# Optimization experiments

Measured on AMD Instinct MI355X. Metric: run time of the kernel, lower is better.

Reference implementation:

```python
import jax, jax.numpy as jnp
import numpy as np
from jax import lax

SR = 7
HEADS = 8
EPS = 1e-5

def dwconv(x, w):
    # x: [B,C,H,W], w: [C,1,3,3] depthwise
    return lax.conv_general_dilated(x, w, (1, 1), 'SAME',
                                    feature_group_count=x.shape[1],
                                    dimension_numbers=('NCHW', 'OIHW', 'NCHW'))

def bn(x, g, b, m, v):
    # eval-mode BatchNorm2d over channel dim of [B,C,H,W]
    scale = g / jnp.sqrt(v + EPS)
    return x * scale[:, None, None] + (b - m * scale)[:, None, None]

def avgpool(x, k):
    B, C, H, W = x.shape
    return x.reshape(B, C, H // k, k, W // k, k).mean(axis=(3, 5))

def upsample(x, k):
    B, C, H, W = x.shape
    return jax.image.resize(x, (B, C, H * k, W * k), method='bilinear')


def setup_inputs() -> dict:
    key = jax.random.key(0)
    ks = jax.random.split(key, 12)
    B, N, C = 16, 3136, 256
    d = {}
    d['x'] = jax.random.normal(ks[0], (B, N, C), jnp.float32)
    d['Wv'] = jax.random.normal(ks[1], (C, C), jnp.float32) * 0.05
    d['conv1_w'] = jax.random.normal(ks[2], (C, 1, 3, 3), jnp.float32) * 0.05
    d['bn1_g'] = jnp.ones((C,), jnp.float32)
    d['bn1_b'] = jnp.zeros((C,), jnp.float32)
    d['bn1_m'] = jax.random.normal(ks[3], (C,), jnp.float32) * 0.05
    d['bn1_v'] = jax.random.uniform(ks[4], (C,), jnp.float32, 0.5, 1.5)
    d['conv2_w'] = jax.random.normal(ks[5], (C, 1, 3, 3), jnp.float32) * 0.05
    d['bn2_g'] = jnp.ones((C,), jnp.float32)
    d['bn2_b'] = jnp.zeros((C,), jnp.float32)
    d['bn2_m'] = jax.random.normal(ks[6], (C,), jnp.float32) * 0.05
    d['bn2_v'] = jax.random.uniform(ks[7], (C,), jnp.float32, 0.5, 1.5)
    d['vup_w'] = jax.random.normal(ks[8], (C, 1, 3, 3), jnp.float32) * 0.05
    d['bn3_g'] = jnp.ones((C,), jnp.float32)
    d['bn3_b'] = jnp.zeros((C,), jnp.float32)
    d['bn3_m'] = jax.random.normal(ks[9], (C,), jnp.float32) * 0.05
    d['bn3_v'] = jax.random.uniform(ks[10], (C,), jnp.float32, 0.5, 1.5)
    d['Wp'] = jax.random.normal(ks[11], (C, C), jnp.float32) * 0.05
    d['bp'] = jnp.zeros((C,), jnp.float32)
    return d


def reference(x, Wv, conv1_w, bn1_g, bn1_b, bn1_m, bn1_v,
              conv2_w, bn2_g, bn2_b, bn2_m, bn2_v,
              vup_w, bn3_g, bn3_b, bn3_m, bn3_v, Wp, bp):
    B, N, C = x.shape
    h = w = int(np.sqrt(N))
    hd = C // HEADS
    scale = C ** (-0.5)

    v = x @ Wv.T                                    # [B,N,C] (torch Linear, no bias)
    skip = v.reshape(B, h, w, C).transpose(0, 3, 1, 2)  # [B,C,h,w]

    s1 = bn(dwconv(skip, conv1_w), bn1_g, bn1_b, bn1_m, bn1_v)
    q = avgpool(s1, SR)                             # [B,C,h_,w_]
    s2 = bn(dwconv(jax.nn.gelu(s1, approximate=False), conv2_w),
            bn2_g, bn2_b, bn2_m, bn2_v)
    k = avgpool(s2, SR)                             # [B,C,h_,w_]
    skip_tok = jax.nn.gelu(s2, approximate=False).reshape(B, C, N).transpose(0, 2, 1)

    h_, w_ = h // SR, w // SR
    N_ = h_ * w_
    qh = q.reshape(B, HEADS, hd, N_).transpose(0, 1, 3, 2)   # [B,H,N_,d]
    kh = k.reshape(B, HEADS, hd, N_).transpose(0, 1, 3, 2)   # [B,H,N_,d]
    vh = v.reshape(B, N, HEADS, hd).transpose(0, 2, 1, 3)    # [B,H,N,d]

    attn = jnp.einsum('bhnd,bhmd->bhnm', qh, kh)             # [B,H,N_,N_]
    attn = attn.reshape(B * HEADS, N_, h_, w_)
    attn = upsample(attn, SR) * scale                        # [B*H,N_,h,w]
    attn = attn.reshape(B, HEADS, N_, N)
    attn = jax.nn.softmax(attn, axis=-1)

    o = jnp.einsum('bhnm,bhmd->bhnd', attn, vh)              # [B,H,N_,d]
    o = o.reshape(B, HEADS, h_, w_, hd).transpose(0, 1, 4, 2, 3).reshape(B, C, h_, w_)
    o = bn(dwconv(upsample(o, SR), vup_w), bn3_g, bn3_b, bn3_m, bn3_v)  # [B,C,h,w]

    out = o.reshape(B, C, N).transpose(0, 2, 1) + skip_tok
    out = out @ Wp.T + bp
    return out
```

## Files before the change

### kernel.cpp

```cpp
#include <hip/hip_runtime.h>
#include <math.h>

#define B_     16
#define H_IMG  56
#define W_IMG  56
#define N_TOK  3136
#define C_     256
#define C4_    64
#define NHEAD  8
#define HDIM   32
#define NCH    8

typedef float f32x4 __attribute__((ext_vector_type(4)));
typedef __bf16 bf16x8 __attribute__((ext_vector_type(8)));

__device__ __forceinline__ float geluf(float x) {
    return 0.5f * x * (1.0f + erff(x * 0.70710678118654752f));
}

__device__ __forceinline__ void up_coef(int o, int& i0, int& i1, float& t) {
    float f  = (float)(o - 3) * (1.0f / 7.0f);
    float fl = floorf(f);
    int   ii = (int)fl;
    t = f - fl;
    if (ii < 0)       { i0 = 0; i1 = 0; t = 0.0f; }
    else if (ii >= 7) { i0 = 7; i1 = 7; t = 0.0f; }
    else              { i0 = ii; i1 = ii + 1; }
}

__device__ __forceinline__ void split_bf16(float4 f, uint2& hi, uint2& lo) {
    unsigned u0 = __float_as_uint(f.x), u1 = __float_as_uint(f.y);
    unsigned u2 = __float_as_uint(f.z), u3 = __float_as_uint(f.w);
    unsigned h0 = u0 & 0xFFFF0000u, h1 = u1 & 0xFFFF0000u;
    unsigned h2 = u2 & 0xFFFF0000u, h3 = u3 & 0xFFFF0000u;
    hi = make_uint2((h0 >> 16) | h1, (h2 >> 16) | h3);
    float l0 = f.x - __uint_as_float(h0);
    float l1 = f.y - __uint_as_float(h1);
    float l2 = f.z - __uint_as_float(h2);
    float l3 = f.w - __uint_as_float(h3);
    lo = make_uint2((__float_as_uint(l0) >> 16) | (__float_as_uint(l1) & 0xFFFF0000u),
                    (__float_as_uint(l2) >> 16) | (__float_as_uint(l3) & 0xFFFF0000u));
}

__device__ __forceinline__ unsigned pack2_bf16(float a, float b) {
    __bf16 ha = (__bf16)a, hb = (__bf16)b;
    unsigned short ua = __builtin_bit_cast(unsigned short, ha);
    unsigned short ub = __builtin_bit_cast(unsigned short, hb);
    return (unsigned)ua | ((unsigned)ub << 16);
}

__device__ __forceinline__ void gload_lds16(const float* g, float* l) {
    __builtin_amdgcn_global_load_lds(
        (const __attribute__((address_space(1))) unsigned int*)g,
        (__attribute__((address_space(3))) unsigned int*)l, 16, 0, 0);
}

__global__ void prep_kernel(
    const float* __restrict__ w1, const float* __restrict__ w2, const float* __restrict__ w3,
    const float* __restrict__ g1, const float* __restrict__ b1, const float* __restrict__ m1, const float* __restrict__ v1,
    const float* __restrict__ g2, const float* __restrict__ b2, const float* __restrict__ m2, const float* __restrict__ v2,
    const float* __restrict__ g3, const float* __restrict__ b3, const float* __restrict__ m3, const float* __restrict__ v3,
    float* __restrict__ wT1, float* __restrict__ wT2, float* __restrict__ wT3,
    float* __restrict__ sc1, float* __restrict__ sh1,
    float* __restrict__ sc2, float* __restrict__ sh2,
    float* __restrict__ sc3, float* __restrict__ sh3)
{
    int c = threadIdx.x;
#pragma unroll
    for (int t = 0; t < 9; ++t) {
        wT1[t * C_ + c] = w1[c * 9 + t];
        wT2[t * C_ + c] = w2[c * 9 + t];
        wT3[t * C_ + c] = w3[c * 9 + t];
    }
    float s1 = g1[c] * rsqrtf(v1[c] + 1e-5f); sc1[c] = s1; sh1[c] = b1[c] - m1[c] * s1;
    float s2 = g2[c] * rsqrtf(v2[c] + 1e-5f); sc2[c] = s2; sh2[c] = b2[c] - m2[c] * s2;
    float s3 = g3[c] * rsqrtf(v3[c] + 1e-5f); sc3[c] = s3; sh3[c] = b3[c] - m3[c] * s3;
}

__global__ __launch_bounds__(256, 2) void gemm_nt_mfma_kernel(
    const float* __restrict__ A,
    const float* __restrict__ Bm,
    const float* __restrict__ bias,
    float* __restrict__ C,
    int M, int N)
{
    __shared__ float lds[8192];
    const int tid  = threadIdx.x;
    const int nb   = N >> 7;
    const int nwg  = (M >> 7) * nb;
    const int cpx  = nwg >> 3;
    const int bid  = blockIdx.x;
    const int swz  = (bid & 7) * cpx + (bid >> 3);
    const int bx   = swz % nb;
    const int by   = swz / nb;
    const int lane = tid & 63;
    const int wv   = tid >> 6;
    const int wr   = wv >> 1, wc = wv & 1;
    const int l15  = lane & 15, kb = lane >> 4;

    const float* Abase = A  + (size_t)(by * 128) * 256;
    const float* Bbase = Bm + (size_t)(bx * 128) * 256;

    f32x4 acc[4][4];
#pragma unroll
    for (int m = 0; m < 4; ++m)
#pragma unroll
        for (int n = 0; n < 4; ++n) acc[m][n] = (f32x4)(0.0f);

    int srow[4], ssk[4];
#pragma unroll
    for (int i = 0; i < 4; ++i) {
        int u = i * 256 + tid;
        srow[i] = u >> 3;
        ssk[i]  = ((u & 7) ^ (srow[i] & 7)) << 2;
    }

#pragma unroll
    for (int k0 = 0; k0 < 256; k0 += 32) {
        __syncthreads();
#pragma unroll
        for (int i = 0; i < 4; ++i) {
            int u = i * 256 + tid;
            gload_lds16(Abase + (size_t)srow[i] * 256 + k0 + ssk[i], &lds[u * 4]);
        }
#pragma unroll
        for (int i = 0; i < 4; ++i) {
            int u = i * 256 + tid;
            gload_lds16(Bbase + (size_t)srow[i] * 256 + k0 + ssk[i], &lds[4096 + u * 4]);
        }
        __syncthreads();

        bf16x8 ah[4], al[4], bh[4], bl[4];
#pragma unroll
        for (int m = 0; m < 4; ++m) {
            int r = wr * 64 + m * 16 + l15;
            float4 f0 = *(const float4*)&lds[r * 32 + ((((kb * 2)    ) ^ (r & 7)) << 2)];
            float4 f1 = *(const float4*)&lds[r * 32 + ((((kb * 2) + 1) ^ (r & 7)) << 2)];
            uint2 h0, l0, h1, l1;
            split_bf16(f0, h0, l0);
            split_bf16(f1, h1, l1);
            ah[m] = __builtin_bit_cast(bf16x8, make_uint4(h0.x, h0.y, h1.x, h1.y));
            al[m] = __builtin_bit_cast(bf16x8, make_uint4(l0.x, l0.y, l1.x, l1.y));
        }
#pragma unroll
        for (int n = 0; n < 4; ++n) {
            int r = wc * 64 + n * 16 + l15;
            float4 f0 = *(const float4*)&lds[4096 + r * 32 + ((((kb * 2)    ) ^ (r & 7)) << 2)];
            float4 f1 = *(const float4*)&lds[4096 + r * 32 + ((((kb * 2) + 1) ^ (r & 7)) << 2)];
            uint2 h0, l0, h1, l1;
            split_bf16(f0, h0, l0);
            split_bf16(f1, h1, l1);
            bh[n] = __builtin_bit_cast(bf16x8, make_uint4(h0.x, h0.y, h1.x, h1.y));
            bl[n] = __builtin_bit_cast(bf16x8, make_uint4(l0.x, l0.y, l1.x, l1.y));
        }
#pragma unroll
        for (int m = 0; m < 4; ++m)
#pragma unroll
            for (int n = 0; n < 4; ++n) {
                acc[m][n] = __builtin_amdgcn_mfma_f32_16x16x32_bf16(ah[m], bh[n], acc[m][n], 0, 0, 0);
                acc[m][n] = __builtin_amdgcn_mfma_f32_16x16x32_bf16(ah[m], bl[n], acc[m][n], 0, 0, 0);
                acc[m][n] = __builtin_amdgcn_mfma_f32_16x16x32_bf16(al[m], bh[n], acc[m][n], 0, 0, 0);
            }
    }

    const int rb = by * 128 + wr * 64 + kb * 4;
    const int cb = bx * 128 + wc * 64 + l15;
#pragma unroll
    for (int n = 0; n < 4; ++n) {
        int col = cb + n * 16;
        float bv = bias ? bias[col] : 0.0f;
#pragma unroll
        for (int m = 0; m < 4; ++m) {
            int row = rb + m * 16;
#pragma unroll
            for (int r = 0; r < 4; ++r)
                C[(size_t)(row + r) * N + col] = acc[m][n][r] + bv;
        }
    }
}

__global__ __launch_bounds__(256, 4) void dwconv_bn_pool_gelu_kernel(
    const float* __restrict__ in, const float* __restrict__ wT,
    const float* __restrict__ scv, const float* __restrict__ shv,
    float* __restrict__ outg, float* __restrict__ pool)
{
    const int blk = blockIdx.x;
    const int xcd = blk & 7;
    const int j   = blk >> 3;
    const int b   = xcd + 8 * (j >> 6);
    const int g   = j & 63;
    const int gy  = g >> 3, gx = g & 7;
    const int tid = threadIdx.x;
    const int c4  = tid & 63;
    const int wv  = tid >> 6;
    const int c0  = c4 * 4;

    float4 wr[9];
#pragma unroll
    for (int t = 0; t < 9; ++t) wr[t] = *(const float4*)(wT + t * C_ + c0);
    const float4 sc = *(const float4*)(scv + c0);
    const float4 sh = *(const float4*)(shv + c0);

    const int x0 = gx * 7, y0 = gy * 7;
    const float* inb = in + (size_t)b * N_TOK * C_;
    float4 acc = make_float4(0, 0, 0, 0);

    for (int p = wv; p < 49; p += 4) {
        int py = p / 7, px = p - py * 7;
        int y = y0 + py, x = x0 + px;
        float cx = 0.f, cy = 0.f, cz = 0.f, cw = 0.f;
#pragma unroll
        for (int dy = -1; dy <= 1; ++dy) {
            int yy = y + dy;
            if (yy < 0 || yy >= H_IMG) continue;
#pragma unroll
            for (int dx = -1; dx <= 1; ++dx) {
                int xx = x + dx;
                if (xx < 0 || xx >= W_IMG) continue;
                const float4 iv = *(const float4*)(inb + (size_t)(yy * W_IMG + xx) * C_ + c0);
                const float4 w  = wr[(dy + 1) * 3 + (dx + 1)];
                cx = fmaf(iv.x, w.x, cx);
                cy = fmaf(iv.y, w.y, cy);
                cz = fmaf(iv.z, w.z, cz);
                cw = fmaf(iv.w, w.w, cw);
            }
        }
        float vx = cx * sc.x + sh.x;
        float vy = cy * sc.y + sh.y;
        float vz = cz * sc.z + sh.z;
        float vw = cw * sc.w + sh.w;
        acc.x += vx; acc.y += vy; acc.z += vz; acc.w += vw;
        *(float4*)(outg + ((size_t)b * N_TOK + y * W_IMG + x) * C_ + c0) =
            make_float4(geluf(vx), geluf(vy), geluf(vz), geluf(vw));
    }

    __shared__ float4 ps[4][64];
    ps[wv][c4] = acc;
    __syncthreads();
    if (tid < 64) {
        float4 s  = ps[0][tid];
        float4 t1 = ps[1][tid];
        float4 t2 = ps[2][tid];
        float4 t3 = ps[3][tid];
        const float r = 1.0f / 49.0f;
        *(float4*)(pool + ((size_t)b * 64 + g) * C_ + tid * 4) = make_float4(
            (s.x + t1.x + t2.x + t3.x) * r, (s.y + t1.y + t2.y + t3.y) * r,
            (s.z + t1.z + t2.z + t3.z) * r, (s.w + t1.w + t2.w + t3.w) * r);
    }
}

__global__ __launch_bounds__(256, 3) void dwconv_up_bn_add_kernel(
    const float* __restrict__ osm,
    const float* __restrict__ wT,
    const float* __restrict__ scv, const float* __restrict__ shv,
    const float* __restrict__ add_,
    float* __restrict__ out)
{
    const int blk = blockIdx.x;
    const int xcd = blk & 7;
    const int j   = blk >> 3;
    const int b   = xcd + 8 * (j >> 6);
    const int g   = j & 63;
    const int gy  = g >> 3, gx = g & 7;
    const int tid = threadIdx.x;
    const int c4  = tid & 63;
    const int wv  = tid >> 6;
    const int c0  = c4 * 4;

    float4 wr[9];
#pragma unroll
    for (int t = 0; t < 9; ++t) wr[t] = *(const float4*)(wT + t * C_ + c0);
    const float4 sc = *(const float4*)(scv + c0);
    const float4 sh = *(const float4*)(shv + c0);

    const float* ob = osm + (size_t)b * 64 * C_ + c0;
    const int cry0 = max(gy - 1, 0), cry2 = min(gy + 1, 7);
    const int crx0 = max(gx - 1, 0), crx2 = min(gx + 1, 7);
    float4 P[3][3];
#pragma unroll
    for (int ri = 0; ri < 3; ++ri) {
        const int rowc = (ri == 0) ? cry0 : ((ri == 1) ? gy : cry2);
        P[ri][0] = *(const float4*)(ob + (size_t)(rowc * 8 + crx0) * C_);
        P[ri][1] = *(const float4*)(ob + (size_t)(rowc * 8 + gx)   * C_);
        P[ri][2] = *(const float4*)(ob + (size_t)(rowc * 8 + crx2) * C_);
    }

    for (int cpass = 0; cpass < 2; ++cpass) {
        const int xi = wv + cpass * 4;
        if (xi >= 7) break;
        const int x = gx * 7 + xi;

        float axw[3][3];
#pragma unroll
        for (int e = 0; e < 3; ++e) {
            int xx = x - 1 + e;
            if (xx >= 0 && xx < W_IMG) {
                int i0, i1; float t;
                up_coef(xx, i0, i1, t);
                const bool r0 = (i0 - gx + 1) == 0;
                axw[e][0] = r0 ? (1.0f - t) : 0.0f;
                axw[e][1] = r0 ? t : (1.0f - t);
                axw[e][2] = r0 ? 0.0f : t;
            } else {
                axw[e][0] = 0.0f; axw[e][1] = 0.0f; axw[e][2] = 0.0f;
            }
        }

        float4 S[3][3];
#pragma unroll
        for (int d = 0; d < 3; ++d) {
            float4 cw0, cw1, cw2;
#pragma unroll
            for (int ci = 0; ci < 3; ++ci) {
                float4 c;
                c.x = wr[d*3+0].x * axw[0][ci] + wr[d*3+1].x * axw[1][ci] + wr[d*3+2].x * axw[2][ci];
                c.y = wr[d*3+0].y * axw[0][ci] + wr[d*3+1].y * axw[1][ci] + wr[d*3+2].y * axw[2][ci];
                c.z = wr[d*3+0].z * axw[0][ci] + wr[d*3+1].z * axw[1][ci] + wr[d*3+2].z * axw[2][ci];
                c.w = wr[d*3+0].w * axw[0][ci] + wr[d*3+1].w * axw[1][ci] + wr[d*3+2].w * axw[2][ci];
                if (ci == 0) cw0 = c; else if (ci == 1) cw1 = c; else cw2 = c;
            }
#pragma unroll
            for (int ri = 0; ri < 3; ++ri) {
                float4 s;
                s.x = cw0.x * P[ri][0].x + cw1.x * P[ri][1].x + cw2.x * P[ri][2].x;
                s.y = cw0.y * P[ri][0].y + cw1.y * P[ri][1].y + cw2.y * P[ri][2].y;
                s.z = cw0.z * P[ri][0].z + cw1.z * P[ri][1].z + cw2.z * P[ri][2].z;
                s.w = cw0.w * P[ri][0].w + cw1.w * P[ri][1].w + cw2.w * P[ri][2].w;
                S[d][ri] = s;
            }
        }

#pragma unroll
        for (int y7 = 0; y7 < 7; ++y7) {
            const int y = gy * 7 + y7;
            float ax = 0.f, ay = 0.f, az = 0.f, aw = 0.f;
#pragma unroll
            for (int d = 0; d < 3; ++d) {
                const int yy = y + d - 1;
                if (yy < 0 || yy >= H_IMG) continue;
                int i0, i1; float ty;
                up_coef(yy, i0, i1, ty);
                const bool hi2 = (i0 - gy + 1) != 0;
                const float4 lo = hi2 ? S[d][1] : S[d][0];
                const float4 hi = hi2 ? S[d][2] : S[d][1];
                ax += fmaf(ty, hi.x - lo.x, lo.x);
                ay += fmaf(ty, hi.y - lo.y, lo.y);
                az += fmaf(ty, hi.z - lo.z, lo.z);
                aw += fmaf(ty, hi.w - lo.w, lo.w);
            }
            const size_t pix = (size_t)b * N_TOK + (size_t)y * W_IMG + x;
            const float4 av = *(const float4*)(add_ + pix * C_ + c0);
            *(float4*)(out + pix * C_ + c0) = make_float4(
                ax * sc.x + sh.x + av.x, ay * sc.y + sh.y + av.y,
                az * sc.z + sh.z + av.z, aw * sc.w + sh.w + av.w);
        }
    }
}

__global__ __launch_bounds__(256) void qk_kernel(
    const float* __restrict__ q, const float* __restrict__ k,
    float* __restrict__ attnL, float* __restrict__ mrow_g)
{
    int bh = blockIdx.x;
    int b = bh >> 3, head = bh & 7;
    __shared__ float qs[64][33];
    __shared__ float ks[64][33];
    int tid = threadIdx.x;
    for (int t = tid; t < 512; t += 256) {
        int i = t >> 3, dq = (t & 7) * 4;
        const float4 qv = *(const float4*)(q + ((size_t)(b * 64 + i) * C_ + head * 32 + dq));
        const float4 kv = *(const float4*)(k + ((size_t)(b * 64 + i) * C_ + head * 32 + dq));
        qs[i][dq + 0] = qv.x; qs[i][dq + 1] = qv.y; qs[i][dq + 2] = qv.z; qs[i][dq + 3] = qv.w;
        ks[i][dq + 0] = kv.x; ks[i][dq + 1] = kv.y; ks[i][dq + 2] = kv.z; ks[i][dq + 3] = kv.w;
    }
    __syncthreads();
    int i  = tid >> 2;
    int jb = (tid & 3) * 16;
    float qr[32];
#pragma unroll
    for (int d = 0; d < 32; ++d) qr[d] = qs[i][d];
    float* outp = attnL + (size_t)bh * 4096 + i * 64 + jb;
    float mloc = -1e30f;
#pragma unroll
    for (int j = 0; j < 16; ++j) {
        float s = 0.f;
#pragma unroll
        for (int d = 0; d < 32; ++d) s = fmaf(qr[d], ks[jb + j][d], s);
        float sv = s * 0.0625f;
        outp[j] = sv;
        mloc = fmaxf(mloc, sv);
    }
    mloc = fmaxf(mloc, __shfl_xor(mloc, 1));
    mloc = fmaxf(mloc, __shfl_xor(mloc, 2));
    if ((tid & 3) == 0) mrow_g[bh * 64 + i] = mloc;
}

#define S_ALS 0
#define S_P   1792
#define S_VH  4096
#define S_VL  5248
#define S_RY  6400
#define S_ZP  7168
__global__ __launch_bounds__(256, 4) void attn_pv_kernel(
    const float* __restrict__ attnL,
    const float* __restrict__ mrow_g,
    const float* __restrict__ v,
    float* __restrict__ part_o,
    float* __restrict__ part_z)
{
    __shared__ unsigned sm[7424];
    float* smf = (float*)sm;

    const int blk   = blockIdx.x;
    const int xcd   = blk & 7;
    const int r8    = blk >> 3;
    const int b     = xcd + 8 * (r8 >> 6);
    const int rem   = r8 & 63;
    const int head  = rem >> 3;
    const int chunk = rem & 7;
    const int bh    = b * 8 + head;
    const int jb    = min(max(chunk - 1, 0), 5);

    const int tid  = threadIdx.x;
    const int lane = tid & 63;
    const int w    = tid >> 6;
    const int l15  = lane & 15, kb = lane >> 4;
    const int i    = tid >> 2;
    const int dg   = tid & 3;

    for (int u = tid; u < 384; u += 256) {
        int row = u / 6, cc = u % 6;
        float4 va = *(const float4*)(attnL + (size_t)bh * 4096 + row * 64 + jb * 8 + cc * 4);
        *(float4*)&smf[S_ALS + row * 28 + cc * 4] = va;
    }
    sm[S_P + (tid >> 2) * 36 + 28 + (tid & 3)] = 0;
    {
        int base = (tid < 128) ? S_VH : S_VL;
        int q2 = tid & 127;
        sm[base + (q2 >> 2) * 36 + 28 + (q2 & 3)] = 0;
    }
    const float mr = mrow_g[bh * 64 + i];

    int   x0a[14]; float txa[14];
#pragma unroll
    for (int j = 0; j < 14; ++j) {
        int i0, i1; float t;
        up_coef(dg * 14 + j, i0, i1, t);
        x0a[j] = i0; txa[j] = t;
    }

    f32x4 acc[2];
    acc[0] = (f32x4)(0.0f); acc[1] = (f32x4)(0.0f);
    float zacc = 0.0f;

    for (int rr = 0; rr < 7; ++rr) {
        const int y = chunk * 7 + rr;
        __syncthreads();

        float4 va, vb;
        if (tid < 224) {
            int x2 = tid >> 3, d0 = (tid & 7) * 4;
            const float* vp = v + ((size_t)b * N_TOK + y * W_IMG + 2 * x2) * C_ + head * 32 + d0;
            va = *(const float4*)vp;
            vb = *(const float4*)(vp + C_);
        }
        {
            int y0, y1; float ty;
            up_coef(y, y0, y1, ty);
#pragma unroll
            for (int kk2 = dg; kk2 < 9; kk2 += 4) {
                int ks2 = kk2 < 8 ? kk2 : 7;
                float a0 = smf[S_ALS + i * 28 + (y0 - jb) * 8 + ks2];
                float a1 = smf[S_ALS + i * 28 + (y1 - jb) * 8 + ks2];
                smf[S_RY + i * 12 + kk2] = fmaf(ty, a1 - a0, a0) - mr;
            }
        }
        if (tid < 224) {
            int x2 = tid >> 3, d0 = (tid & 7) * 4;
            float ae[4] = {va.x, va.y, va.z, va.w};
            float be[4] = {vb.x, vb.y, vb.z, vb.w};
#pragma unroll
            for (int j = 0; j < 4; ++j) {
                unsigned ua = __float_as_uint(ae[j]), ha = ua & 0xFFFF0000u;
                unsigned ub = __float_as_uint(be[j]), hb2 = ub & 0xFFFF0000u;
                sm[S_VH + (d0 + j) * 36 + x2] = (ha >> 16) | hb2;
                float la = ae[j] - __uint_as_float(ha);
                float lb = be[j] - __uint_as_float(hb2);
                sm[S_VL + (d0 + j) * 36 + x2] =
                    (__float_as_uint(la) >> 16) | (__float_as_uint(lb) & 0xFFFF0000u);
            }
        }
        __syncthreads();

#pragma unroll
        for (int j = 0; j < 7; ++j) {
            float r0 = smf[S_RY + i * 12 + x0a[2 * j]];
            float r1 = smf[S_RY + i * 12 + x0a[2 * j] + 1];
            float l0 = fmaf(txa[2 * j], r1 - r0, r0);
            float r2 = smf[S_RY + i * 12 + x0a[2 * j + 1]];
            float r3 = smf[S_RY + i * 12 + x0a[2 * j + 1] + 1];
            float l1 = fmaf(txa[2 * j + 1], r3 - r2, r2);
            float p0 = __expf(l0), p1 = __expf(l1);
            zacc += p0 + p1;
            sm[S_P + i * 36 + dg * 7 + j] = pack2_bf16(p0, p1);
        }
        __syncthreads();

#pragma unroll
        for (int s = 0; s < 2; ++s) {
            bf16x8 pa = *(const bf16x8*)&sm[S_P + (w * 16 + l15) * 36 + s * 16 + kb * 4];
#pragma unroll
            for (int n = 0; n < 2; ++n) {
                bf16x8 bhv = *(const bf16x8*)&sm[S_VH + (n * 16 + l15) * 36 + s * 16 + kb * 4];
                bf16x8 blv = *(const bf16x8*)&sm[S_VL + (n * 16 + l15) * 36 + s * 16 + kb * 4];
                acc[n] = __builtin_amdgcn_mfma_f32_16x16x32_bf16(pa, bhv, acc[n], 0, 0, 0);
                acc[n] = __builtin_amdgcn_mfma_f32_16x16x32_bf16(pa, blv, acc[n], 0, 0, 0);
            }
        }
    }

    smf[S_ZP + i * 4 + dg] = zacc;
    __syncthreads();
    if (tid < 64) {
        float zt = smf[S_ZP + tid * 4] + smf[S_ZP + tid * 4 + 1] +
                   smf[S_ZP + tid * 4 + 2] + smf[S_ZP + tid * 4 + 3];
        part_z[((size_t)bh * NCH + chunk) * 64 + tid] = zt;
    }
    const int row4 = (lane >> 4) * 4;
#pragma unroll
    for (int n = 0; n < 2; ++n)
#pragma unroll
        for (int r2 = 0; r2 < 4; ++r2) {
            int i2 = w * 16 + row4 + r2;
            int d  = n * 16 + l15;
            part_o[(((size_t)bh * NCH + chunk) * 64 + i2) * 32 + d] = acc[n][r2];
        }
}

__global__ __launch_bounds__(256) void combine_kernel(
    const float* __restrict__ part_o, const float* __restrict__ part_z,
    float* __restrict__ o_small)
{
    int idx = blockIdx.x * 256 + threadIdx.x;
    if (idx >= B_ * 64 * C_) return;
    int c = idx % C_;
    int g = (idx / C_) % 64;
    int b = idx / (C_ * 64);
    int head = c >> 5, d = c & 31;
    int bh = b * 8 + head;
    float oo = 0.f, zz = 0.f;
    for (int ch = 0; ch < NCH; ++ch) {
        oo += part_o[(((size_t)bh * NCH + ch) * 64 + g) * 32 + d];
        zz += part_z[((size_t)bh * NCH + ch) * 64 + g];
    }
    o_small[idx] = oo / zz;
}

extern "C" void kernel_launch(void* const* d_in, const int* in_sizes, int n_in,
                              void* d_out, int out_size, void* d_ws, size_t ws_size,
                              hipStream_t stream)
{
    const float* x    = (const float*)d_in[0];
    const float* Wv   = (const float*)d_in[1];
    const float* c1w  = (const float*)d_in[2];
    const float* b1g  = (const float*)d_in[3];
    const float* b1b  = (const float*)d_in[4];
    const float* b1m  = (const float*)d_in[5];
    const float* b1v  = (const float*)d_in[6];
    const float* c2w  = (const float*)d_in[7];
    const float* b2g  = (const float*)d_in[8];
    const float* b2b  = (const float*)d_in[9];
    const float* b2m  = (const float*)d_in[10];
    const float* b2v  = (const float*)d_in[11];
    const float* vupw = (const float*)d_in[12];
    const float* b3g  = (const float*)d_in[13];
    const float* b3b  = (const float*)d_in[14];
    const float* b3m  = (const float*)d_in[15];
    const float* b3v  = (const float*)d_in[16];
    const float* Wp   = (const float*)d_in[17];
    const float* bp   = (const float*)d_in[18];
    float* out = (float*)d_out;
    float* ws  = (float*)d_ws;

    const size_t SZ = (size_t)B_ * N_TOK * C_;
    float* v       = ws;
    float* s1g     = v   + SZ;
    float* s2g     = s1g + SZ;
    float* q       = s2g + SZ;
    float* kk      = q  + (size_t)B_ * 64 * C_;
    float* attnL   = kk + (size_t)B_ * 64 * C_;
    float* part_o  = attnL  + (size_t)B_ * 8 * 64 * 64;
    float* part_z  = part_o + (size_t)B_ * 8 * NCH * 64 * 32;
    float* o_small = part_z + (size_t)B_ * 8 * NCH * 64;
    float* wT1     = o_small + (size_t)B_ * 64 * C_;
    float* wT2     = wT1 + 9 * C_;
    float* wT3     = wT2 + 9 * C_;
    float* sc1     = wT3 + 9 * C_;
    float* sh1     = sc1 + C_;
    float* sc2     = sh1 + C_;
    float* sh2     = sc2 + C_;
    float* sc3     = sh2 + C_;
    float* sh3     = sc3 + C_;
    float* mrow_g  = sh3 + C_;

    const int M = B_ * N_TOK;

    prep_kernel<<<1, 256, 0, stream>>>(c1w, c2w, vupw,
        b1g, b1b, b1m, b1v, b2g, b2b, b2m, b2v, b3g, b3b, b3m, b3v,
        wT1, wT2, wT3, sc1, sh1, sc2, sh2, sc3, sh3);
    gemm_nt_mfma_kernel<<<(M / 128) * (C_ / 128), 256, 0, stream>>>(x, Wv, nullptr, v, M, C_);
    dwconv_bn_pool_gelu_kernel<<<1024, 256, 0, stream>>>(v, wT1, sc1, sh1, s1g, q);
    dwconv_bn_pool_gelu_kernel<<<1024, 256, 0, stream>>>(s1g, wT2, sc2, sh2, s2g, kk);
    qk_kernel<<<B_ * 8, 256, 0, stream>>>(q, kk, attnL, mrow_g);
    attn_pv_kernel<<<B_ * 8 * NCH, 256, 0, stream>>>(attnL, mrow_g, v, part_o, part_z);
    combine_kernel<<<B_ * 64 * C_ / 256, 256, 0, stream>>>(part_o, part_z, o_small);
    dwconv_up_bn_add_kernel<<<1024, 256, 0, stream>>>(o_small, wT3, sc3, sh3, s2g, v);
    gemm_nt_mfma_kernel<<<(M / 128) * (C_ / 128), 256, 0, stream>>>(v, Wp, bp, out, M, C_);
}
```

Before: 211.3 us.

## Fuse both depthwise conv stages into one kernel with halo recompute in LDS

Replaces the two separate dwconv+BN+pool+GELU launches with one kernel. Each block computes the first conv over a 9x9 halo tile, keeps gelu(s1) in shared memory, then runs the second conv from LDS. This removes the global write and re-read of the intermediate s1 tensor and one launch. In exchange it recomputes halo pixels (81 vs 49 per tile), splits channels into two halves per block, and adds about 42KB of LDS per block, which can limit occupancy.

```diff
diff --git a/kernel.cpp b/kernel.cpp
--- a/kernel.cpp
+++ b/kernel.cpp
@@ -78,11 +78,8 @@
 }
 
 __global__ __launch_bounds__(256, 2) void gemm_nt_mfma_kernel(
-    const float* __restrict__ A,
-    const float* __restrict__ Bm,
-    const float* __restrict__ bias,
-    float* __restrict__ C,
-    int M, int N)
+    const float* __restrict__ A, const float* __restrict__ Bm,
+    const float* __restrict__ bias, float* __restrict__ C, int M, int N)
 {
     __shared__ float lds[8192];
     const int tid  = threadIdx.x;
@@ -179,82 +176,136 @@
     }
 }
 
-__global__ __launch_bounds__(256, 4) void dwconv_bn_pool_gelu_kernel(
-    const float* __restrict__ in, const float* __restrict__ wT,
-    const float* __restrict__ scv, const float* __restrict__ shv,
-    float* __restrict__ outg, float* __restrict__ pool)
-{
+__global__ __launch_bounds__(256, 3) void dwconv12_fused_kernel(
+    const float* __restrict__ v,
+    const float* __restrict__ wT1, const float* __restrict__ sc1v, const float* __restrict__ sh1v,
+    const float* __restrict__ wT2, const float* __restrict__ sc2v, const float* __restrict__ sh2v,
+    float* __restrict__ s2g,
+    float* __restrict__ qpool,
+    float* __restrict__ kpool)
+{
+    __shared__ float4 sg[81 * 33];
+    __shared__ float4 ps[8][32];
+
     const int blk = blockIdx.x;
     const int xcd = blk & 7;
     const int j   = blk >> 3;
-    const int b   = xcd + 8 * (j >> 6);
-    const int g   = j & 63;
+    const int b   = xcd + 8 * (j >> 7);
+    const int rem = j & 127;
+    const int g   = rem >> 1;
+    const int ch  = rem & 1;
     const int gy  = g >> 3, gx = g & 7;
     const int tid = threadIdx.x;
-    const int c4  = tid & 63;
-    const int wv  = tid >> 6;
-    const int c0  = c4 * 4;
-
-    float4 wr[9];
-#pragma unroll
-    for (int t = 0; t < 9; ++t) wr[t] = *(const float4*)(wT + t * C_ + c0);
-    const float4 sc = *(const float4*)(scv + c0);
-    const float4 sh = *(const float4*)(shv + c0);
-
-    const int x0 = gx * 7, y0 = gy * 7;
-    const float* inb = in + (size_t)b * N_TOK * C_;
-    float4 acc = make_float4(0, 0, 0, 0);
-
-    for (int p = wv; p < 49; p += 4) {
-        int py = p / 7, px = p - py * 7;
-        int y = y0 + py, x = x0 + px;
+    const int q32 = tid & 31;
+    const int slot = tid >> 5;
+    const int c0  = ch * 128 + q32 * 4;
+
+    float4 w1r[9], w2r[9];
+#pragma unroll
+    for (int t = 0; t < 9; ++t) {
+        w1r[t] = *(const float4*)(wT1 + t * C_ + c0);
+        w2r[t] = *(const float4*)(wT2 + t * C_ + c0);
+    }
+    const float4 sc1 = *(const float4*)(sc1v + c0);
+    const float4 sh1 = *(const float4*)(sh1v + c0);
+    const float4 sc2 = *(const float4*)(sc2v + c0);
+    const float4 sh2 = *(const float4*)(sh2v + c0);
+
+    const int y0 = gy * 7, x0 = gx * 7;
+    const float* inb = v + (size_t)b * N_TOK * C_;
+    float4 qacc = make_float4(0, 0, 0, 0);
+
+    for (int p = slot; p < 81; p += 8) {
+        int py = p / 9, px = p - py * 9;
+        int y = y0 - 1 + py, x = x0 - 1 + px;
+        float4 o = make_float4(0, 0, 0, 0);
+        if (y >= 0 && y < H_IMG && x >= 0 && x < W_IMG) {
+            float cx = 0.f, cy = 0.f, cz = 0.f, cw = 0.f;
+#pragma unroll
+            for (int dy = -1; dy <= 1; ++dy) {
+                int yy = y + dy;
+                if (yy < 0 || yy >= H_IMG) continue;
+#pragma unroll
+                for (int dx = -1; dx <= 1; ++dx) {
+                    int xx = x + dx;
+                    if (xx < 0 || xx >= W_IMG) continue;
+                    const float4 iv = *(const float4*)(inb + (size_t)(yy * W_IMG + xx) * C_ + c0);
+                    const float4 w  = w1r[(dy + 1) * 3 + (dx + 1)];
+                    cx = fmaf(iv.x, w.x, cx);
+                    cy = fmaf(iv.y, w.y, cy);
+                    cz = fmaf(iv.z, w.z, cz);
+                    cw = fmaf(iv.w, w.w, cw);
+                }
+            }
+            float s1x = cx * sc1.x + sh1.x;
+            float s1y = cy * sc1.y + sh1.y;
+            float s1z = cz * sc1.z + sh1.z;
+            float s1w = cw * sc1.w + sh1.w;
+            if (py >= 1 && py <= 7 && px >= 1 && px <= 7) {
+                qacc.x += s1x; qacc.y += s1y; qacc.z += s1z; qacc.w += s1w;
+            }
+            o = make_float4(geluf(s1x), geluf(s1y), geluf(s1z), geluf(s1w));
+        }
+        sg[p * 33 + q32] = o;
+    }
+    ps[slot][q32] = qacc;
+    __syncthreads();
+
+    if (tid < 32) {
+        float4 s = ps[0][tid];
+#pragma unroll
+        for (int t = 1; t < 8; ++t) {
+            float4 u = ps[t][tid];
+            s.x += u.x; s.y += u.y; s.z += u.z; s.w += u.w;
+        }
+        const float r = 1.0f / 49.0f;
+        *(float4*)(qpool + ((size_t)b * 64 + g) * C_ + ch * 128 + tid * 4) =
+            make_float4(s.x * r, s.y * r, s.z * r, s.w * r);
+    }
+
+    float4 kacc = make_float4(0, 0, 0, 0);
+    for (int p2 = slot; p2 < 49; p2 += 8) {
+        int qy = p2 / 7, qx = p2 - qy * 7;
         float cx = 0.f, cy = 0.f, cz = 0.f, cw = 0.f;
 #pragma unroll
-        for (int dy = -1; dy <= 1; ++dy) {
-            int yy = y + dy;
-            if (yy < 0 || yy >= H_IMG) continue;
-#pragma unroll
-            for (int dx = -1; dx <= 1; ++dx) {
-                int xx = x + dx;
-                if (xx < 0 || xx >= W_IMG) continue;
-                const float4 iv = *(const float4*)(inb + (size_t)(yy * W_IMG + xx) * C_ + c0);
-                const float4 w  = wr[(dy + 1) * 3 + (dx + 1)];
-                cx = fmaf(iv.x, w.x, cx);
-                cy = fmaf(iv.y, w.y, cy);
-                cz = fmaf(iv.z, w.z, cz);
-                cw = fmaf(iv.w, w.w, cw);
-            }
-        }
-        float vx = cx * sc.x + sh.x;
-        float vy = cy * sc.y + sh.y;
-        float vz = cz * sc.z + sh.z;
-        float vw = cw * sc.w + sh.w;
-        acc.x += vx; acc.y += vy; acc.z += vz; acc.w += vw;
-        *(float4*)(outg + ((size_t)b * N_TOK + y * W_IMG + x) * C_ + c0) =
-            make_float4(geluf(vx), geluf(vy), geluf(vz), geluf(vw));
-    }
-
-    __shared__ float4 ps[4][64];
-    ps[wv][c4] = acc;
+        for (int dy = 0; dy < 3; ++dy)
+#pragma unroll
+            for (int dx = 0; dx < 3; ++dx) {
+                const float4 t4 = sg[((qy + dy) * 9 + (qx + dx)) * 33 + q32];
+                const float4 w  = w2r[dy * 3 + dx];
+                cx = fmaf(t4.x, w.x, cx);
+                cy = fmaf(t4.y, w.y, cy);
+                cz = fmaf(t4.z, w.z, cz);
+                cw = fmaf(t4.w, w.w, cw);
+            }
+        float s2x = cx * sc2.x + sh2.x;
+        float s2y = cy * sc2.y + sh2.y;
+        float s2z = cz * sc2.z + sh2.z;
+        float s2w = cw * sc2.w + sh2.w;
+        kacc.x += s2x; kacc.y += s2y; kacc.z += s2z; kacc.w += s2w;
+        *(float4*)(s2g + ((size_t)b * N_TOK + (y0 + qy) * W_IMG + (x0 + qx)) * C_ + c0) =
+            make_float4(geluf(s2x), geluf(s2y), geluf(s2z), geluf(s2w));
+    }
     __syncthreads();
-    if (tid < 64) {
-        float4 s  = ps[0][tid];
-        float4 t1 = ps[1][tid];
-        float4 t2 = ps[2][tid];
-        float4 t3 = ps[3][tid];
+    ps[slot][q32] = kacc;
+    __syncthreads();
+    if (tid < 32) {
+        float4 s = ps[0][tid];
+#pragma unroll
+        for (int t = 1; t < 8; ++t) {
+            float4 u = ps[t][tid];
+            s.x += u.x; s.y += u.y; s.z += u.z; s.w += u.w;
+        }
         const float r = 1.0f / 49.0f;
-        *(float4*)(pool + ((size_t)b * 64 + g) * C_ + tid * 4) = make_float4(
-            (s.x + t1.x + t2.x + t3.x) * r, (s.y + t1.y + t2.y + t3.y) * r,
-            (s.z + t1.z + t2.z + t3.z) * r, (s.w + t1.w + t2.w + t3.w) * r);
+        *(float4*)(kpool + ((size_t)b * 64 + g) * C_ + ch * 128 + tid * 4) =
+            make_float4(s.x * r, s.y * r, s.z * r, s.w * r);
     }
 }
 
 __global__ __launch_bounds__(256, 3) void dwconv_up_bn_add_kernel(
-    const float* __restrict__ osm,
-    const float* __restrict__ wT,
+    const float* __restrict__ osm, const float* __restrict__ wT,
     const float* __restrict__ scv, const float* __restrict__ shv,
-    const float* __restrict__ add_,
-    float* __restrict__ out)
+    const float* __restrict__ add_, float* __restrict__ out)
 {
     const int blk = blockIdx.x;
     const int xcd = blk & 7;
@@ -609,8 +660,7 @@
         b1g, b1b, b1m, b1v, b2g, b2b, b2m, b2v, b3g, b3b, b3m, b3v,
         wT1, wT2, wT3, sc1, sh1, sc2, sh2, sc3, sh3);
     gemm_nt_mfma_kernel<<<(M / 128) * (C_ / 128), 256, 0, stream>>>(x, Wv, nullptr, v, M, C_);
-    dwconv_bn_pool_gelu_kernel<<<1024, 256, 0, stream>>>(v, wT1, sc1, sh1, s1g, q);
-    dwconv_bn_pool_gelu_kernel<<<1024, 256, 0, stream>>>(s1g, wT2, sc2, sh2, s2g, kk);
+    dwconv12_fused_kernel<<<2048, 256, 0, stream>>>(v, wT1, sc1, sh1, wT2, sc2, sh2, s2g, q, kk);
     qk_kernel<<<B_ * 8, 256, 0, stream>>>(q, kk, attnL, mrow_g);
     attn_pv_kernel<<<B_ * 8 * NCH, 256, 0, stream>>>(attnL, mrow_g, v, part_o, part_z);
     combine_kernel<<<B_ * 64 * C_ / 256, 256, 0, stream>>>(part_o, part_z, o_small);
```

New measurement: 206.4 us. 2.3% less time.
